# Optimization experiments

Measured on AMD Instinct MI355X. Metric: run time of the kernel, lower is better.

Reference implementation:

```python
import jax, jax.numpy as jnp
import numpy as np

B, C, D, TOPK = 4096, 8192, 128, 10


def calc_distmat2(x, y):
    d = (x * x).sum(-1)[:, None] + (y * y).sum(-1)[None, :] - 2.0 * (x @ y.T)
    return jnp.clip(d, 1e-12, 1e12)


def setup_inputs() -> dict:
    key = jax.random.key(0)
    k1, k2, k3 = jax.random.split(key, 3)
    x = jax.random.normal(k1, (B, D), dtype=jnp.float32)
    labels = jax.random.randint(k2, (B,), 0, C)
    # kaiming_normal_(mode='fan_out') on (C, D): fan_out = C, gain = sqrt(2)
    centers = jax.random.normal(k3, (C, D), dtype=jnp.float32) * np.float32(np.sqrt(2.0 / C))
    return {"x": x, "labels": labels, "centers": centers, "topk": TOPK}


def reference(x, labels, centers, topk):
    num_classes = centers.shape[0]
    distmat = calc_distmat2(x, centers)                      # (B, C)
    lab = labels[:, None]                                    # (B, 1)
    dist_pull = jnp.take_along_axis(distmat, lab, axis=1)[:, 0]  # (B,)
    loss_pull = dist_pull.mean()

    # mode 'exp': per-row masked topk over negatives + log-softmax over [pos, neg_topk]
    logits = -distmat                                        # (B, C)
    pos = jnp.take_along_axis(logits, lab, axis=1)           # (B, 1)
    is_pos = lab == jnp.arange(num_classes)[None, :]         # (B, C)
    neg_logits = jnp.where(is_pos, -jnp.inf, logits)
    neg_topk, _ = jax.lax.top_k(neg_logits, topk)            # (B, topk)
    cat = jnp.concatenate([pos, neg_topk], axis=1)           # (B, 1+topk)
    # -log_softmax at index 0 (the positive) per row, averaged ('ccent')
    loss = (-jax.nn.log_softmax(cat, axis=1)[:, 0]).mean()

    # center-to-center repulsion over strictly-lower-triangular pairs
    cent2cent = calc_distmat2(centers, centers)              # (C, C)
    tri = jnp.tril(jnp.ones((num_classes, num_classes), dtype=bool), -1)
    n_pairs = num_classes * (num_classes - 1) // 2
    loss_dis = -jnp.sum(jnp.where(tri, cent2cent, 0.0)) / jnp.float32(n_pairs)

    return (loss, loss_dis, cent2cent, loss_pull)
```

## Files before the change

### kernel.cpp

```cpp
#include <hip/hip_runtime.h>
#include <hip/hip_bf16.h>
#include <math.h>

#define NB 4096
#define NC 8192
#define ND 128
#define NSPLIT 16
#define CPS (NC / NSPLIT)
#define NTILES (CPS / 16)

#define WS_XN 16
#define WS_CN (WS_XN + NB)
#define WS_POS (WS_CN + NC)
#define WS_PART (WS_POS + NB)
#define WS_XB (WS_PART + NB * NSPLIT * 10)
#define WS_CB (WS_XB + NB * ND / 2)

typedef __attribute__((ext_vector_type(8))) short short8v;
typedef __attribute__((ext_vector_type(4))) float f32x4;

__global__ void init_ws_kernel(float* ws) {
  if (threadIdx.x < 16) ws[threadIdx.x] = 0.0f;
}

__global__ __launch_bounds__(256) void prep_kernel(
    const float* __restrict__ x, const float* __restrict__ c, float* __restrict__ ws) {
  int wid = threadIdx.x >> 6, lane = threadIdx.x & 63;
  int row = blockIdx.x * 4 + wid;
  const float* src;
  float* ndst;
  ushort* bdst;
  if (row < NB) {
    src = x + (size_t)row * ND;
    ndst = ws + WS_XN + row;
    bdst = (ushort*)(ws + WS_XB) + (size_t)row * ND;
  } else {
    int r = row - NB;
    src = c + (size_t)r * ND;
    ndst = ws + WS_CN + r;
    bdst = (ushort*)(ws + WS_CB) + (size_t)r * ND;
  }
  float2 v = *(const float2*)(src + lane * 2);
  __hip_bfloat16 h0 = __float2bfloat16(v.x);
  __hip_bfloat16 h1 = __float2bfloat16(v.y);
  ushort2 u;
  u.x = *(ushort*)&h0;
  u.y = *(ushort*)&h1;
  *(ushort2*)(bdst + lane * 2) = u;
  float s = fmaf(v.x, v.x, v.y * v.y);
#pragma unroll
  for (int off = 32; off; off >>= 1) s += __shfl_down(s, off, 64);
  if (lane == 0) *ndst = s;
}

#define INS10(arr, val)                          \
  {                                              \
    float _v = (val);                            \
    _Pragma("unroll") for (int _k = 0; _k < 10; ++_k) { \
      float _mx = fmaxf(arr[_k], _v);            \
      _v = fminf(arr[_k], _v);                   \
      arr[_k] = _mx;                             \
    }                                            \
  }

__global__ __launch_bounds__(256) void xloss_kernel(
    const int* __restrict__ labels, float* __restrict__ ws) {
  int t = threadIdx.x;
  int w = t >> 6, l = t & 63;
  int lo = l & 15, hi = l >> 4;
  int row = blockIdx.x * 64 + w * 16 + lo;
  int split = blockIdx.y;
  int cbase = split * CPS;

  const ushort* xb = (const ushort*)(ws + WS_XB);
  const ushort* cb = (const ushort*)(ws + WS_CB);

  const ushort* xrp = xb + (size_t)row * ND + hi * 8;
  short8v xf0 = *(const short8v*)(xrp + 0);
  short8v xf1 = *(const short8v*)(xrp + 32);
  short8v xf2 = *(const short8v*)(xrp + 64);
  short8v xf3 = *(const short8v*)(xrp + 96);

  float xn = ws[WS_XN + row];
  int lab = labels[row];

  float top[10];
#pragma unroll
  for (int k = 0; k < 10; ++k) top[k] = -3.0e38f;
  float posv = -3.0e38f;

  for (int tl = 0; tl < NTILES; ++tl) {
    int c0 = cbase + tl * 16;
    const ushort* cp = cb + (size_t)(c0 + lo) * ND + hi * 8;
    short8v a0 = *(const short8v*)(cp + 0);
    short8v a1 = *(const short8v*)(cp + 32);
    short8v a2 = *(const short8v*)(cp + 64);
    short8v a3 = *(const short8v*)(cp + 96);
    f32x4 acc = {0.f, 0.f, 0.f, 0.f};
    acc = __builtin_amdgcn_mfma_f32_16x16x32_bf16(a0, xf0, acc, 0, 0, 0);
    acc = __builtin_amdgcn_mfma_f32_16x16x32_bf16(a1, xf1, acc, 0, 0, 0);
    acc = __builtin_amdgcn_mfma_f32_16x16x32_bf16(a2, xf2, acc, 0, 0, 0);
    acc = __builtin_amdgcn_mfma_f32_16x16x32_bf16(a3, xf3, acc, 0, 0, 0);

    f32x4 cn4 = *(const f32x4*)(ws + WS_CN + c0 + hi * 4);
#pragma unroll
    for (int r = 0; r < 4; ++r) {
      int cidx = c0 + hi * 4 + r;
      float dist = xn + cn4[r] - 2.0f * acc[r];
      dist = fminf(fmaxf(dist, 1e-12f), 1e12f);
      float s = -dist;
      bool isl = (cidx == lab);
      posv = isl ? s : posv;
      float se = isl ? -3.0e38f : s;
      INS10(top, se)
    }
  }

  float oth[10];
#pragma unroll
  for (int m = 16; m <= 32; m <<= 1) {
#pragma unroll
    for (int k = 0; k < 10; ++k) oth[k] = __shfl_xor(top[k], m, 64);
#pragma unroll
    for (int k = 0; k < 10; ++k) INS10(top, oth[k])
  }

  if (posv > -1.0e37f) ws[WS_POS + row] = posv;
  if (hi == 0) {
    float* dst = ws + WS_PART + ((size_t)row * NSPLIT + split) * 10;
#pragma unroll
    for (int k = 0; k < 10; ++k) dst[k] = top[k];
  }
}

__global__ __launch_bounds__(256) void merge_kernel(float* __restrict__ ws) {
  int row = blockIdx.x * 256 + threadIdx.x;
  const f32x4* part = (const f32x4*)(ws + WS_PART + (size_t)row * NSPLIT * 10);
  float top[10];
#pragma unroll
  for (int k = 0; k < 10; ++k) top[k] = -3.0e38f;
#pragma unroll
  for (int i = 0; i < NSPLIT * 10 / 4; ++i) {
    f32x4 v = part[i];
    INS10(top, v.x)
    INS10(top, v.y)
    INS10(top, v.z)
    INS10(top, v.w)
  }
  float pos = ws[WS_POS + row];
  float mx = fmaxf(pos, top[0]);
  float ssum = expf(pos - mx);
#pragma unroll
  for (int k = 0; k < 10; ++k) ssum += expf(top[k] - mx);
  float lrow = mx + logf(ssum) - pos;
  float prow = -pos;
#pragma unroll
  for (int off = 32; off; off >>= 1) {
    lrow += __shfl_down(lrow, off, 64);
    prow += __shfl_down(prow, off, 64);
  }
  if ((threadIdx.x & 63) == 0) {
    atomicAdd(ws + 0, lrow);
    atomicAdd(ws + 2, prow);
  }
}

__global__ __launch_bounds__(256) void c2c_kernel(
    float* __restrict__ ws, float* __restrict__ outmat) {
  int bi = blockIdx.x, bj = blockIdx.y;
  int t = threadIdx.x;
  int w = t >> 6, l = t & 63, lo = l & 15, hi = l >> 4;
  int wm = w >> 1, wn = w & 1;
  int rowb = bi * 128 + wm * 64;
  int colb = bj * 128 + wn * 64;
  const ushort* cb = (const ushort*)(ws + WS_CB);

  f32x4 acc[4][4];
#pragma unroll
  for (int m = 0; m < 4; ++m)
#pragma unroll
    for (int n = 0; n < 4; ++n) acc[m][n] = (f32x4){0.f, 0.f, 0.f, 0.f};

#pragma unroll
  for (int ks = 0; ks < 4; ++ks) {
    short8v af[4], bf[4];
#pragma unroll
    for (int m = 0; m < 4; ++m)
      af[m] = *(const short8v*)(cb + (size_t)(rowb + m * 16 + lo) * ND + ks * 32 + hi * 8);
#pragma unroll
    for (int n = 0; n < 4; ++n)
      bf[n] = *(const short8v*)(cb + (size_t)(colb + n * 16 + lo) * ND + ks * 32 + hi * 8);
#pragma unroll
    for (int m = 0; m < 4; ++m)
#pragma unroll
      for (int n = 0; n < 4; ++n)
        acc[m][n] = __builtin_amdgcn_mfma_f32_16x16x32_bf16(af[m], bf[n], acc[m][n], 0, 0, 0);
  }

  float cnj[4];
#pragma unroll
  for (int n = 0; n < 4; ++n) cnj[n] = ws[WS_CN + colb + n * 16 + lo];
  float tsum = 0.0f;
#pragma unroll
  for (int m = 0; m < 4; ++m) {
    f32x4 cni = *(const f32x4*)(ws + WS_CN + rowb + m * 16 + hi * 4);
#pragma unroll
    for (int n = 0; n < 4; ++n) {
#pragma unroll
      for (int rr = 0; rr < 4; ++rr) {
        int gr = rowb + m * 16 + hi * 4 + rr;
        int gc = colb + n * 16 + lo;
        float dd = cni[rr] + cnj[n] - 2.0f * acc[m][n][rr];
        dd = fminf(fmaxf(dd, 1e-12f), 1e12f);
        outmat[(size_t)gr * NC + gc] = dd;
        if (bi > bj) tsum += dd;
        else if (bi == bj) tsum += (gr > gc) ? dd : 0.0f;
      }
    }
  }

  __shared__ float red[4];
#pragma unroll
  for (int off = 32; off; off >>= 1) tsum += __shfl_down(tsum, off, 64);
  if (l == 0) red[w] = tsum;
  __syncthreads();
  if (t == 0) atomicAdd(ws + 1, red[0] + red[1] + red[2] + red[3]);
}

__global__ void finalize_kernel(const float* __restrict__ ws, float* __restrict__ out) {
  if (threadIdx.x == 0) {
    out[0] = ws[0] / 4096.0f;
    out[1] = -ws[1] / 33550336.0f;
    out[2 + (size_t)NC * NC] = ws[2] / 4096.0f;
  }
}

extern "C" void kernel_launch(void* const* d_in, const int* in_sizes, int n_in,
                              void* d_out, int out_size, void* d_ws, size_t ws_size,
                              hipStream_t stream) {
  const float* x = (const float*)d_in[0];
  const int* labels = (const int*)d_in[1];
  const float* centers = (const float*)d_in[2];
  float* out = (float*)d_out;
  float* ws = (float*)d_ws;

  hipLaunchKernelGGL(init_ws_kernel, dim3(1), dim3(64), 0, stream, ws);
  hipLaunchKernelGGL(prep_kernel, dim3((NB + NC) / 4), dim3(256), 0, stream, x, centers, ws);
  hipLaunchKernelGGL(c2c_kernel, dim3(64, 64), dim3(256), 0, stream, ws, out + 2);
  hipLaunchKernelGGL(xloss_kernel, dim3(64, NSPLIT), dim3(256), 0, stream, labels, ws);
  hipLaunchKernelGGL(merge_kernel, dim3(NB / 256), dim3(256), 0, stream, ws);
  hipLaunchKernelGGL(finalize_kernel, dim3(1), dim3(64), 0, stream, ws, out);
}
```

Before: 185.5 us.

## Merge c2c and xloss into one launch, fold init and finalize into neighbors

Combines the center-to-center GEMM kernel and the x-vs-centers top-k kernel into one kernel whose blocks branch on block index, so the two independent workloads can overlap on the GPU. Zeroing the workspace moves into prep_kernel, and finalization moves into the merge kernel through a last-block atomic ticket counter. This cuts six launches to three and removes tail gaps between kernels. The costs are higher register pressure from the fused kernel, which takes the maximum of both branches and may lower occupancy, plus reliance on atomic ordering for the final reduction.

Result: no change. 182.9 us (-1.4%).

```diff
diff --git a/kernel.cpp b/kernel.cpp
--- a/kernel.cpp
+++ b/kernel.cpp
@@ -8,6 +8,7 @@
 #define NSPLIT 16
 #define CPS (NC / NSPLIT)
 #define NTILES (CPS / 16)
+#define XBLKS (64 * NSPLIT)
 
 #define WS_XN 16
 #define WS_CN (WS_XN + NB)
@@ -19,12 +20,9 @@
 typedef __attribute__((ext_vector_type(8))) short short8v;
 typedef __attribute__((ext_vector_type(4))) float f32x4;
 
-__global__ void init_ws_kernel(float* ws) {
-  if (threadIdx.x < 16) ws[threadIdx.x] = 0.0f;
-}
-
 __global__ __launch_bounds__(256) void prep_kernel(
     const float* __restrict__ x, const float* __restrict__ c, float* __restrict__ ws) {
+  if (blockIdx.x == 0 && threadIdx.x < 16) ws[threadIdx.x] = 0.0f;
   int wid = threadIdx.x >> 6, lane = threadIdx.x & 63;
   int row = blockIdx.x * 4 + wid;
   const float* src;
@@ -63,77 +61,138 @@
     }                                            \
   }
 
-__global__ __launch_bounds__(256) void xloss_kernel(
-    const int* __restrict__ labels, float* __restrict__ ws) {
+__global__ __launch_bounds__(256) void mega_kernel(
+    const int* __restrict__ labels, float* __restrict__ ws, float* __restrict__ outmat) {
   int t = threadIdx.x;
-  int w = t >> 6, l = t & 63;
-  int lo = l & 15, hi = l >> 4;
-  int row = blockIdx.x * 64 + w * 16 + lo;
-  int split = blockIdx.y;
-  int cbase = split * CPS;
-
-  const ushort* xb = (const ushort*)(ws + WS_XB);
-  const ushort* cb = (const ushort*)(ws + WS_CB);
-
-  const ushort* xrp = xb + (size_t)row * ND + hi * 8;
-  short8v xf0 = *(const short8v*)(xrp + 0);
-  short8v xf1 = *(const short8v*)(xrp + 32);
-  short8v xf2 = *(const short8v*)(xrp + 64);
-  short8v xf3 = *(const short8v*)(xrp + 96);
-
-  float xn = ws[WS_XN + row];
-  int lab = labels[row];
-
-  float top[10];
-#pragma unroll
-  for (int k = 0; k < 10; ++k) top[k] = -3.0e38f;
-  float posv = -3.0e38f;
-
-  for (int tl = 0; tl < NTILES; ++tl) {
-    int c0 = cbase + tl * 16;
-    const ushort* cp = cb + (size_t)(c0 + lo) * ND + hi * 8;
-    short8v a0 = *(const short8v*)(cp + 0);
-    short8v a1 = *(const short8v*)(cp + 32);
-    short8v a2 = *(const short8v*)(cp + 64);
-    short8v a3 = *(const short8v*)(cp + 96);
-    f32x4 acc = {0.f, 0.f, 0.f, 0.f};
-    acc = __builtin_amdgcn_mfma_f32_16x16x32_bf16(a0, xf0, acc, 0, 0, 0);
-    acc = __builtin_amdgcn_mfma_f32_16x16x32_bf16(a1, xf1, acc, 0, 0, 0);
-    acc = __builtin_amdgcn_mfma_f32_16x16x32_bf16(a2, xf2, acc, 0, 0, 0);
-    acc = __builtin_amdgcn_mfma_f32_16x16x32_bf16(a3, xf3, acc, 0, 0, 0);
-
-    f32x4 cn4 = *(const f32x4*)(ws + WS_CN + c0 + hi * 4);
-#pragma unroll
-    for (int r = 0; r < 4; ++r) {
-      int cidx = c0 + hi * 4 + r;
-      float dist = xn + cn4[r] - 2.0f * acc[r];
-      dist = fminf(fmaxf(dist, 1e-12f), 1e12f);
-      float s = -dist;
-      bool isl = (cidx == lab);
-      posv = isl ? s : posv;
-      float se = isl ? -3.0e38f : s;
-      INS10(top, se)
-    }
-  }
-
-  float oth[10];
-#pragma unroll
-  for (int m = 16; m <= 32; m <<= 1) {
-#pragma unroll
-    for (int k = 0; k < 10; ++k) oth[k] = __shfl_xor(top[k], m, 64);
-#pragma unroll
-    for (int k = 0; k < 10; ++k) INS10(top, oth[k])
-  }
-
-  if (posv > -1.0e37f) ws[WS_POS + row] = posv;
-  if (hi == 0) {
-    float* dst = ws + WS_PART + ((size_t)row * NSPLIT + split) * 10;
-#pragma unroll
-    for (int k = 0; k < 10; ++k) dst[k] = top[k];
-  }
-}
-
-__global__ __launch_bounds__(256) void merge_kernel(float* __restrict__ ws) {
+  int w = t >> 6, l = t & 63, lo = l & 15, hi = l >> 4;
+  int bid = blockIdx.x;
+
+  if (bid < XBLKS) {
+    int split = bid >> 6;
+    int row = (bid & 63) * 64 + w * 16 + lo;
+    int cbase = split * CPS;
+    const ushort* xb = (const ushort*)(ws + WS_XB);
+    const ushort* cb = (const ushort*)(ws + WS_CB);
+
+    const ushort* xrp = xb + (size_t)row * ND + hi * 8;
+    short8v xf0 = *(const short8v*)(xrp + 0);
+    short8v xf1 = *(const short8v*)(xrp + 32);
+    short8v xf2 = *(const short8v*)(xrp + 64);
+    short8v xf3 = *(const short8v*)(xrp + 96);
+
+    float xn = ws[WS_XN + row];
+    int lab = labels[row];
+
+    float top[10];
+#pragma unroll
+    for (int k = 0; k < 10; ++k) top[k] = -3.0e38f;
+    float posv = -3.0e38f;
+
+    for (int tl = 0; tl < NTILES; ++tl) {
+      int c0 = cbase + tl * 16;
+      const ushort* cp = cb + (size_t)(c0 + lo) * ND + hi * 8;
+      short8v a0 = *(const short8v*)(cp + 0);
+      short8v a1 = *(const short8v*)(cp + 32);
+      short8v a2 = *(const short8v*)(cp + 64);
+      short8v a3 = *(const short8v*)(cp + 96);
+      f32x4 acc = {0.f, 0.f, 0.f, 0.f};
+      acc = __builtin_amdgcn_mfma_f32_16x16x32_bf16(a0, xf0, acc, 0, 0, 0);
+      acc = __builtin_amdgcn_mfma_f32_16x16x32_bf16(a1, xf1, acc, 0, 0, 0);
+      acc = __builtin_amdgcn_mfma_f32_16x16x32_bf16(a2, xf2, acc, 0, 0, 0);
+      acc = __builtin_amdgcn_mfma_f32_16x16x32_bf16(a3, xf3, acc, 0, 0, 0);
+
+      f32x4 cn4 = *(const f32x4*)(ws + WS_CN + c0 + hi * 4);
+#pragma unroll
+      for (int r = 0; r < 4; ++r) {
+        int cidx = c0 + hi * 4 + r;
+        float dist = xn + cn4[r] - 2.0f * acc[r];
+        dist = fminf(fmaxf(dist, 1e-12f), 1e12f);
+        float s = -dist;
+        bool isl = (cidx == lab);
+        posv = isl ? s : posv;
+        float se = isl ? -3.0e38f : s;
+        INS10(top, se)
+      }
+    }
+
+    float oth[10];
+#pragma unroll
+    for (int m = 16; m <= 32; m <<= 1) {
+#pragma unroll
+      for (int k = 0; k < 10; ++k) oth[k] = __shfl_xor(top[k], m, 64);
+#pragma unroll
+      for (int k = 0; k < 10; ++k) INS10(top, oth[k])
+    }
+
+    if (posv > -1.0e37f) ws[WS_POS + row] = posv;
+    if (hi == 0) {
+      float* dst = ws + WS_PART + ((size_t)row * NSPLIT + split) * 10;
+#pragma unroll
+      for (int k = 0; k < 10; ++k) dst[k] = top[k];
+    }
+  } else {
+    int bid2 = bid - XBLKS;
+    int bi = bid2 >> 6, bj = bid2 & 63;
+    int wm = w >> 1, wn = w & 1;
+    int rowb = bi * 128 + wm * 64;
+    int colb = bj * 128 + wn * 64;
+    const ushort* cb = (const ushort*)(ws + WS_CB);
+
+    f32x4 acc[4][4];
+#pragma unroll
+    for (int m = 0; m < 4; ++m)
+#pragma unroll
+      for (int n = 0; n < 4; ++n) acc[m][n] = (f32x4){0.f, 0.f, 0.f, 0.f};
+
+#pragma unroll
+    for (int ks = 0; ks < 4; ++ks) {
+      short8v af[4], bf[4];
+#pragma unroll
+      for (int m = 0; m < 4; ++m)
+        af[m] = *(const short8v*)(cb + (size_t)(rowb + m * 16 + lo) * ND + ks * 32 + hi * 8);
+#pragma unroll
+      for (int n = 0; n < 4; ++n)
+        bf[n] = *(const short8v*)(cb + (size_t)(colb + n * 16 + lo) * ND + ks * 32 + hi * 8);
+#pragma unroll
+      for (int m = 0; m < 4; ++m)
+#pragma unroll
+        for (int n = 0; n < 4; ++n)
+          acc[m][n] = __builtin_amdgcn_mfma_f32_16x16x32_bf16(af[m], bf[n], acc[m][n], 0, 0, 0);
+    }
+
+    float cnj[4];
+#pragma unroll
+    for (int n = 0; n < 4; ++n) cnj[n] = ws[WS_CN + colb + n * 16 + lo];
+    float tsum = 0.0f;
+#pragma unroll
+    for (int m = 0; m < 4; ++m) {
+      f32x4 cni = *(const f32x4*)(ws + WS_CN + rowb + m * 16 + hi * 4);
+#pragma unroll
+      for (int n = 0; n < 4; ++n) {
+#pragma unroll
+        for (int rr = 0; rr < 4; ++rr) {
+          int gr = rowb + m * 16 + hi * 4 + rr;
+          int gc = colb + n * 16 + lo;
+          float dd = cni[rr] + cnj[n] - 2.0f * acc[m][n][rr];
+          dd = fminf(fmaxf(dd, 1e-12f), 1e12f);
+          outmat[(size_t)gr * NC + gc] = dd;
+          if (bi > bj) tsum += dd;
+          else if (bi == bj) tsum += (gr > gc) ? dd : 0.0f;
+        }
+      }
+    }
+
+    __shared__ float red[4];
+#pragma unroll
+    for (int off = 32; off; off >>= 1) tsum += __shfl_down(tsum, off, 64);
+    if (l == 0) red[w] = tsum;
+    __syncthreads();
+    if (t == 0) atomicAdd(ws + 1, red[0] + red[1] + red[2] + red[3]);
+  }
+}
+
+__global__ __launch_bounds__(256) void merge_fin_kernel(float* __restrict__ ws,
+                                                        float* __restrict__ out) {
   int row = blockIdx.x * 256 + threadIdx.x;
   const f32x4* part = (const f32x4*)(ws + WS_PART + (size_t)row * NSPLIT * 10);
   float top[10];
@@ -163,75 +222,18 @@
     atomicAdd(ws + 0, lrow);
     atomicAdd(ws + 2, prow);
   }
-}
-
-__global__ __launch_bounds__(256) void c2c_kernel(
-    float* __restrict__ ws, float* __restrict__ outmat) {
-  int bi = blockIdx.x, bj = blockIdx.y;
-  int t = threadIdx.x;
-  int w = t >> 6, l = t & 63, lo = l & 15, hi = l >> 4;
-  int wm = w >> 1, wn = w & 1;
-  int rowb = bi * 128 + wm * 64;
-  int colb = bj * 128 + wn * 64;
-  const ushort* cb = (const ushort*)(ws + WS_CB);
-
-  f32x4 acc[4][4];
-#pragma unroll
-  for (int m = 0; m < 4; ++m)
-#pragma unroll
-    for (int n = 0; n < 4; ++n) acc[m][n] = (f32x4){0.f, 0.f, 0.f, 0.f};
-
-#pragma unroll
-  for (int ks = 0; ks < 4; ++ks) {
-    short8v af[4], bf[4];
-#pragma unroll
-    for (int m = 0; m < 4; ++m)
-      af[m] = *(const short8v*)(cb + (size_t)(rowb + m * 16 + lo) * ND + ks * 32 + hi * 8);
-#pragma unroll
-    for (int n = 0; n < 4; ++n)
-      bf[n] = *(const short8v*)(cb + (size_t)(colb + n * 16 + lo) * ND + ks * 32 + hi * 8);
-#pragma unroll
-    for (int m = 0; m < 4; ++m)
-#pragma unroll
-      for (int n = 0; n < 4; ++n)
-        acc[m][n] = __builtin_amdgcn_mfma_f32_16x16x32_bf16(af[m], bf[n], acc[m][n], 0, 0, 0);
-  }
-
-  float cnj[4];
-#pragma unroll
-  for (int n = 0; n < 4; ++n) cnj[n] = ws[WS_CN + colb + n * 16 + lo];
-  float tsum = 0.0f;
-#pragma unroll
-  for (int m = 0; m < 4; ++m) {
-    f32x4 cni = *(const f32x4*)(ws + WS_CN + rowb + m * 16 + hi * 4);
-#pragma unroll
-    for (int n = 0; n < 4; ++n) {
-#pragma unroll
-      for (int rr = 0; rr < 4; ++rr) {
-        int gr = rowb + m * 16 + hi * 4 + rr;
-        int gc = colb + n * 16 + lo;
-        float dd = cni[rr] + cnj[n] - 2.0f * acc[m][n][rr];
-        dd = fminf(fmaxf(dd, 1e-12f), 1e12f);
-        outmat[(size_t)gr * NC + gc] = dd;
-        if (bi > bj) tsum += dd;
-        else if (bi == bj) tsum += (gr > gc) ? dd : 0.0f;
-      }
-    }
-  }
-
-  __shared__ float red[4];
-#pragma unroll
-  for (int off = 32; off; off >>= 1) tsum += __shfl_down(tsum, off, 64);
-  if (l == 0) red[w] = tsum;
   __syncthreads();
-  if (t == 0) atomicAdd(ws + 1, red[0] + red[1] + red[2] + red[3]);
-}
-
-__global__ void finalize_kernel(const float* __restrict__ ws, float* __restrict__ out) {
   if (threadIdx.x == 0) {
-    out[0] = ws[0] / 4096.0f;
-    out[1] = -ws[1] / 33550336.0f;
-    out[2 + (size_t)NC * NC] = ws[2] / 4096.0f;
+    __threadfence();
+    unsigned tk = atomicAdd((unsigned int*)(ws + 3), 1u);
+    if (tk == 15u) {
+      float ls = atomicAdd(ws + 0, 0.0f);
+      float ts = atomicAdd(ws + 1, 0.0f);
+      float ps = atomicAdd(ws + 2, 0.0f);
+      out[0] = ls / 4096.0f;
+      out[1] = -ts / 33550336.0f;
+      out[2 + (size_t)NC * NC] = ps / 4096.0f;
+    }
   }
 }
 
@@ -244,10 +246,7 @@
   float* out = (float*)d_out;
   float* ws = (float*)d_ws;
 
-  hipLaunchKernelGGL(init_ws_kernel, dim3(1), dim3(64), 0, stream, ws);
   hipLaunchKernelGGL(prep_kernel, dim3((NB + NC) / 4), dim3(256), 0, stream, x, centers, ws);
-  hipLaunchKernelGGL(c2c_kernel, dim3(64, 64), dim3(256), 0, stream, ws, out + 2);
-  hipLaunchKernelGGL(xloss_kernel, dim3(64, NSPLIT), dim3(256), 0, stream, labels, ws);
-  hipLaunchKernelGGL(merge_kernel, dim3(NB / 256), dim3(256), 0, stream, ws);
-  hipLaunchKernelGGL(finalize_kernel, dim3(1), dim3(64), 0, stream, ws, out);
-}
+  hipLaunchKernelGGL(mega_kernel, dim3(XBLKS + 64 * 64), dim3(256), 0, stream, labels, ws, out + 2);
+  hipLaunchKernelGGL(merge_fin_kernel, dim3(NB / 256), dim3(256), 0, stream, ws, out);
+}
```
